# Kernel optimization log

Measured on AMD Instinct MI355X. Metric: run time of the kernel, lower is better.

Reference implementation:

```python
import jax, jax.numpy as jnp
import numpy as np

INV2 = 0.5  # product of two 1/sqrt(2) Haar filter taps


def setup_inputs() -> dict:
    key = jax.random.key(0)
    x = jax.random.normal(key, (8, 64, 512, 512), dtype=jnp.float32)
    return {"x": x}


def reference(x):
    # Haar dwt2 (pywt convention, even H/W so no boundary extension matters):
    # per 2x2 block [[a, b], [c, d]] (rows = axis 2, cols = axis 3):
    #   LL (cA) = (a + b + c + d) / 2
    #   LH (cH) = (a + b - c - d) / 2   # detail along rows (axis 2)
    #   HL (cV) = (a - b + c - d) / 2   # detail along cols (axis 3)
    #   HH (cD) = (a - b - c + d) / 2
    B, C, H, W = x.shape
    xb = x.reshape(B, C, H // 2, 2, W // 2, 2)
    a = xb[:, :, :, 0, :, 0]
    b = xb[:, :, :, 0, :, 1]
    c = xb[:, :, :, 1, :, 0]
    d = xb[:, :, :, 1, :, 1]
    LL = (a + b + c + d) * INV2
    LH = (a + b - c - d) * INV2
    HL = (a - b + c - d) * INV2
    HH = (a - b - c + d) * INV2
    return (LL, LH, HL, HH)
```

## Files before the change

### kernel.cpp

```cpp
#include <hip/hip_runtime.h>


#define BB 8
#define CC 64
#define HH_ 512
#define WW_ 512
#define OUTH (HH_ / 2)
#define OUTW (WW_ / 2)

#define NTHREADS (2048 * 256)
#define ITEMS 16

typedef float v4f __attribute__((ext_vector_type(4)));

__global__ __launch_bounds__(256) void haar2x2_kernel(
    const float* __restrict__ x, float* __restrict__ out)
{
    const size_t subband = (size_t)BB * CC * OUTH * OUTW;

    int idx = blockIdx.x * blockDim.x + threadIdx.x;

#pragma unroll 4
    for (int k = 0; k < ITEMS; ++k) {
        int t = idx + k * NTHREADS;
        int img = t >> 14;
        int rem = t & 16383;
        int ho  = rem >> 6;
        int wo  = rem & 63;

        const float* rowbase = x + (size_t)img * HH_ * WW_ + (size_t)(2 * ho) * WW_;
        const v4f* r0p = reinterpret_cast<const v4f*>(rowbase) + wo * 2;
        const v4f* r1p = reinterpret_cast<const v4f*>(rowbase + WW_) + wo * 2;

        v4f r0a = __builtin_nontemporal_load(r0p);
        v4f r0b = __builtin_nontemporal_load(r0p + 1);
        v4f r1a = __builtin_nontemporal_load(r1p);
        v4f r1b = __builtin_nontemporal_load(r1p + 1);

        v4f ll, lh, hl, hh;

        {
            float s0 = r0a.x + r0a.y, d0 = r0a.x - r0a.y;
            float s1 = r1a.x + r1a.y, d1 = r1a.x - r1a.y;
            ll.x = (s0 + s1) * 0.5f; lh.x = (s0 - s1) * 0.5f;
            hl.x = (d0 + d1) * 0.5f; hh.x = (d0 - d1) * 0.5f;
        }
        {
            float s0 = r0a.z + r0a.w, d0 = r0a.z - r0a.w;
            float s1 = r1a.z + r1a.w, d1 = r1a.z - r1a.w;
            ll.y = (s0 + s1) * 0.5f; lh.y = (s0 - s1) * 0.5f;
            hl.y = (d0 + d1) * 0.5f; hh.y = (d0 - d1) * 0.5f;
        }
        {
            float s0 = r0b.x + r0b.y, d0 = r0b.x - r0b.y;
            float s1 = r1b.x + r1b.y, d1 = r1b.x - r1b.y;
            ll.z = (s0 + s1) * 0.5f; lh.z = (s0 - s1) * 0.5f;
            hl.z = (d0 + d1) * 0.5f; hh.z = (d0 - d1) * 0.5f;
        }
        {
            float s0 = r0b.z + r0b.w, d0 = r0b.z - r0b.w;
            float s1 = r1b.z + r1b.w, d1 = r1b.z - r1b.w;
            ll.w = (s0 + s1) * 0.5f; lh.w = (s0 - s1) * 0.5f;
            hl.w = (d0 + d1) * 0.5f; hh.w = (d0 - d1) * 0.5f;
        }

        size_t obase = (size_t)img * OUTH * OUTW + (size_t)ho * OUTW + (size_t)(wo * 4);
        __builtin_nontemporal_store(ll, reinterpret_cast<v4f*>(out + 0 * subband + obase));
        __builtin_nontemporal_store(lh, reinterpret_cast<v4f*>(out + 1 * subband + obase));
        __builtin_nontemporal_store(hl, reinterpret_cast<v4f*>(out + 2 * subband + obase));
        __builtin_nontemporal_store(hh, reinterpret_cast<v4f*>(out + 3 * subband + obase));
    }
}

extern "C" void kernel_launch(void* const* d_in, const int* in_sizes, int n_in,
                              void* d_out, int out_size, void* d_ws, size_t ws_size,
                              hipStream_t stream) {
    const float* x = (const float*)d_in[0];
    float* out = (float*)d_out;

    haar2x2_kernel<<<2048, 256, 0, stream>>>(x, out);
}
```

Measured before the change: 228.2 us.

## Assign one output row per wave with fully coalesced loads and lane-shuffle stores

Measured after the change: 197.2 us. -13.6%, faster.

```diff
diff --git a/kernel.cpp b/kernel.cpp
--- a/kernel.cpp
+++ b/kernel.cpp
@@ -8,67 +8,83 @@
 #define OUTH (HH_ / 2)
 #define OUTW (WW_ / 2)
 
-#define NTHREADS (2048 * 256)
+#define NWAVES 8192
 #define ITEMS 16
 
 typedef float v4f __attribute__((ext_vector_type(4)));
+
+struct H2 { float ux, uy; };
 
 __global__ __launch_bounds__(256) void haar2x2_kernel(
     const float* __restrict__ x, float* __restrict__ out)
 {
     const size_t subband = (size_t)BB * CC * OUTH * OUTW;
 
-    int idx = blockIdx.x * blockDim.x + threadIdx.x;
+    const int wave = (blockIdx.x * blockDim.x + threadIdx.x) >> 6;
+    const int lane = threadIdx.x & 63;
+    const bool odd = (lane & 1) != 0;
+    const int coloff = ((lane & ~1) << 1) + (odd ? 128 : 0);
 
-#pragma unroll 4
     for (int k = 0; k < ITEMS; ++k) {
-        int t = idx + k * NTHREADS;
-        int img = t >> 14;
-        int rem = t & 16383;
-        int ho  = rem >> 6;
-        int wo  = rem & 63;
+        int item = wave + k * NWAVES;
+        int img  = item >> 8;
+        int ho   = item & 255;
 
-        const float* rowbase = x + (size_t)img * HH_ * WW_ + (size_t)(2 * ho) * WW_;
-        const v4f* r0p = reinterpret_cast<const v4f*>(rowbase) + wo * 2;
-        const v4f* r1p = reinterpret_cast<const v4f*>(rowbase + WW_) + wo * 2;
+        const float* rb = x + (size_t)img * (HH_ * WW_) + (size_t)(2 * ho) * WW_;
+        const v4f* p = reinterpret_cast<const v4f*>(rb);
 
-        v4f r0a = __builtin_nontemporal_load(r0p);
-        v4f r0b = __builtin_nontemporal_load(r0p + 1);
-        v4f r1a = __builtin_nontemporal_load(r1p);
-        v4f r1b = __builtin_nontemporal_load(r1p + 1);
+        v4f A0 = p[lane];
+        v4f A1 = p[64 + lane];
+        v4f B0 = p[128 + lane];
+        v4f B1 = p[192 + lane];
 
-        v4f ll, lh, hl, hh;
-
+        float2 u_ll, u_lh, u_hl, u_hh, v_ll, v_lh, v_hl, v_hh;
         {
-            float s0 = r0a.x + r0a.y, d0 = r0a.x - r0a.y;
-            float s1 = r1a.x + r1a.y, d1 = r1a.x - r1a.y;
-            ll.x = (s0 + s1) * 0.5f; lh.x = (s0 - s1) * 0.5f;
-            hl.x = (d0 + d1) * 0.5f; hh.x = (d0 - d1) * 0.5f;
+            float s0 = A0.x + A0.y, d0 = A0.x - A0.y;
+            float s1 = B0.x + B0.y, d1 = B0.x - B0.y;
+            u_ll.x = (s0 + s1) * 0.5f; u_lh.x = (s0 - s1) * 0.5f;
+            u_hl.x = (d0 + d1) * 0.5f; u_hh.x = (d0 - d1) * 0.5f;
+            s0 = A0.z + A0.w; d0 = A0.z - A0.w;
+            s1 = B0.z + B0.w; d1 = B0.z - B0.w;
+            u_ll.y = (s0 + s1) * 0.5f; u_lh.y = (s0 - s1) * 0.5f;
+            u_hl.y = (d0 + d1) * 0.5f; u_hh.y = (d0 - d1) * 0.5f;
         }
         {
-            float s0 = r0a.z + r0a.w, d0 = r0a.z - r0a.w;
-            float s1 = r1a.z + r1a.w, d1 = r1a.z - r1a.w;
-            ll.y = (s0 + s1) * 0.5f; lh.y = (s0 - s1) * 0.5f;
-            hl.y = (d0 + d1) * 0.5f; hh.y = (d0 - d1) * 0.5f;
-        }
-        {
-            float s0 = r0b.x + r0b.y, d0 = r0b.x - r0b.y;
-            float s1 = r1b.x + r1b.y, d1 = r1b.x - r1b.y;
-            ll.z = (s0 + s1) * 0.5f; lh.z = (s0 - s1) * 0.5f;
-            hl.z = (d0 + d1) * 0.5f; hh.z = (d0 - d1) * 0.5f;
-        }
-        {
-            float s0 = r0b.z + r0b.w, d0 = r0b.z - r0b.w;
-            float s1 = r1b.z + r1b.w, d1 = r1b.z - r1b.w;
-            ll.w = (s0 + s1) * 0.5f; lh.w = (s0 - s1) * 0.5f;
-            hl.w = (d0 + d1) * 0.5f; hh.w = (d0 - d1) * 0.5f;
+            float s0 = A1.x + A1.y, d0 = A1.x - A1.y;
+            float s1 = B1.x + B1.y, d1 = B1.x - B1.y;
+            v_ll.x = (s0 + s1) * 0.5f; v_lh.x = (s0 - s1) * 0.5f;
+            v_hl.x = (d0 + d1) * 0.5f; v_hh.x = (d0 - d1) * 0.5f;
+            s0 = A1.z + A1.w; d0 = A1.z - A1.w;
+            s1 = B1.z + B1.w; d1 = B1.z - B1.w;
+            v_ll.y = (s0 + s1) * 0.5f; v_lh.y = (s0 - s1) * 0.5f;
+            v_hl.y = (d0 + d1) * 0.5f; v_hh.y = (d0 - d1) * 0.5f;
         }
 
-        size_t obase = (size_t)img * OUTH * OUTW + (size_t)ho * OUTW + (size_t)(wo * 4);
-        __builtin_nontemporal_store(ll, reinterpret_cast<v4f*>(out + 0 * subband + obase));
-        __builtin_nontemporal_store(lh, reinterpret_cast<v4f*>(out + 1 * subband + obase));
-        __builtin_nontemporal_store(hl, reinterpret_cast<v4f*>(out + 2 * subband + obase));
-        __builtin_nontemporal_store(hh, reinterpret_cast<v4f*>(out + 3 * subband + obase));
+        size_t obase = (size_t)img * (OUTH * OUTW) + (size_t)ho * OUTW + coloff;
+        float* o0 = out + 0 * subband + obase;
+        float* o1 = out + 1 * subband + obase;
+        float* o2 = out + 2 * subband + obase;
+        float* o3 = out + 3 * subband + obase;
+
+        #define EMIT(U, V, DST)                                            \
+        {                                                                  \
+            float sx = odd ? U.x : V.x;                                    \
+            float sy = odd ? U.y : V.y;                                    \
+            float rx = __shfl_xor(sx, 1, 64);                              \
+            float ry = __shfl_xor(sy, 1, 64);                              \
+            v4f o;                                                         \
+            o.x = odd ? rx : U.x;                                          \
+            o.y = odd ? ry : U.y;                                          \
+            o.z = odd ? V.x : rx;                                          \
+            o.w = odd ? V.y : ry;                                          \
+            __builtin_nontemporal_store(o, reinterpret_cast<v4f*>(DST));   \
+        }
+
+        EMIT(u_ll, v_ll, o0);
+        EMIT(u_lh, v_lh, o1);
+        EMIT(u_hl, v_hl, o2);
+        EMIT(u_hh, v_hh, o3);
+        #undef EMIT
     }
 }
 
```
